# Kernel tuning notes

Hardware: AMD Instinct MI355X
Metric: run time of the kernel (lower is better)

Reference implementation:

```python
import jax, jax.numpy as jnp
import numpy as np

B, S, H, DH = 2, 2048, 16, 64
D = H * DH


def setup_inputs() -> dict:
    key = jax.random.key(0)
    ks = jax.random.split(key, 10)
    std = 0.02
    return {
        "hidden_states": jax.random.normal(ks[0], (B, S, D), jnp.float32),
        "mask": jax.random.randint(ks[1], (B, S), 0, 2, jnp.int64 if jax.config.jax_enable_x64 else jnp.int32),
        "Wq": jax.random.normal(ks[2], (D, D), jnp.float32) * std,
        "bq": jnp.zeros((D,), jnp.float32),
        "Wk": jax.random.normal(ks[3], (D, D), jnp.float32) * std,
        "bk": jnp.zeros((D,), jnp.float32),
        "Wv": jax.random.normal(ks[4], (D, D), jnp.float32) * std,
        "bv": jnp.zeros((D,), jnp.float32),
        "Wo": jax.random.normal(ks[5], (D, D), jnp.float32) * std,
        "bo": jnp.zeros((D,), jnp.float32),
    }


def _split_heads(x):
    # (B, S, H*DH) -> (B, H, S, DH)
    b, s, _ = x.shape
    return x.reshape(b, s, H, DH).transpose(0, 2, 1, 3)


def reference(hidden_states, mask, Wq, bq, Wk, bk, Wv, bv, Wo, bo):
    # Linear projections (torch nn.Linear: x @ W.T + b)
    q = _split_heads(hidden_states @ Wq.T + bq)
    k = _split_heads(hidden_states @ Wk.T + bk)
    v = _split_heads(hidden_states @ Wv.T + bv)

    scale = 1.0 / np.sqrt(DH).astype(np.float32)
    scores = jnp.einsum("bhqd,bhkd->bhqk", q, k) * scale  # (B,H,S,S)
    # mask out padded key positions (mask==0 -> -inf), broadcast over heads/queries
    scores = jnp.where(mask[:, None, None, :] == 0, -jnp.inf, scores)
    weights = jax.nn.softmax(scores, axis=-1)

    attended = jnp.einsum("bhqk,bhkd->bhqd", weights, v)  # (B,H,S,DH)
    merged = attended.transpose(0, 2, 1, 3).reshape(hidden_states.shape)  # (B,S,D)
    return merged @ Wo.T + bo
```

## Files before the change

### kernel.cpp

```cpp
#include <hip/hip_runtime.h>
#include <hip/hip_bf16.h>

typedef __bf16 bf16;
typedef __bf16 bf16x4 __attribute__((ext_vector_type(4)));
typedef __bf16 bf16x8 __attribute__((ext_vector_type(8)));
typedef float f32x4 __attribute__((ext_vector_type(4)));

#define B_ 2
#define S_ 2048
#define H_ 16
#define DH_ 64
#define D_ 1024
#define NT_ 4096

#define WAIT_VMCNT0() asm volatile("s_waitcnt vmcnt(0)" ::: "memory")
#define WAIT_LGKM0()  asm volatile("s_waitcnt lgkmcnt(0)" ::: "memory")

__device__ __forceinline__ void gld_lds16(const bf16* g, bf16* l) {
    __builtin_amdgcn_global_load_lds(
        (__attribute__((address_space(1))) void*)g,
        (__attribute__((address_space(3))) void*)l, 16, 0, 0);
}

__global__ __launch_bounds__(256) void cvt_kernel(
    const float* __restrict__ hs,
    const float* __restrict__ Wq, const float* __restrict__ Wk,
    const float* __restrict__ Wv, const float* __restrict__ Wo,
    bf16* __restrict__ hsb, bf16* __restrict__ wqkv, bf16* __restrict__ wob)
{
    int i = (blockIdx.x * 256 + threadIdx.x) * 4;
    const float* src;
    bf16* dst;
    if (i < 4194304) {
        src = hs + i; dst = hsb + i;
    } else if (i < 7340032) {
        int off = i - 4194304;
        int which = off >> 20;
        int within = off & 1048575;
        src = (which == 0 ? Wq : which == 1 ? Wk : Wv) + within;
        dst = wqkv + off;
    } else {
        int off = i - 7340032;
        src = Wo + off; dst = wob + off;
    }
    float4 v = *(const float4*)src;
    bf16x4 o = { (bf16)v.x, (bf16)v.y, (bf16)v.z, (bf16)v.w };
    *(bf16x4*)dst = o;
}

__global__ __launch_bounds__(256, 2) void gemm_bt(
    const bf16* __restrict__ A, const bf16* __restrict__ Bm,
    int mode,
    const float* __restrict__ b0, const float* __restrict__ b1,
    const float* __restrict__ b2,
    bf16* __restrict__ Qo, bf16* __restrict__ Ko, bf16* __restrict__ Vt,
    float* __restrict__ Co)
{
    const int K = 1024;
    __shared__ __attribute__((aligned(16))) bf16 sA[128 * 32];
    __shared__ __attribute__((aligned(16))) bf16 sB[128 * 32];

    int tid = threadIdx.x;
    int wave = tid >> 6, lane = tid & 63;
    int quad = lane >> 4, l16 = lane & 15;
    int m0 = blockIdx.x * 128;
    int n0 = blockIdx.y * 128;
    int wm = (wave & 1) * 64, wn = (wave >> 1) * 64;
    int fs = (l16 >> 1) & 3;

    f32x4 acc[4][4];
#pragma unroll
    for (int i = 0; i < 4; i++)
#pragma unroll
        for (int j = 0; j < 4; j++) acc[i][j] = (f32x4){0.f, 0.f, 0.f, 0.f};

    for (int k0 = 0; k0 < K; k0 += 32) {
#pragma unroll
        for (int i = 0; i < 2; i++) {
            int chunk = tid + i * 256;
            int row = chunk >> 2;
            int kc = ((chunk & 3) ^ ((row >> 1) & 3)) * 8;
            gld_lds16(A + (size_t)(m0 + row) * K + k0 + kc, &sA[chunk * 8]);
            gld_lds16(Bm + (size_t)(n0 + row) * K + k0 + kc, &sB[chunk * 8]);
        }
        WAIT_VMCNT0();
        __syncthreads();

        bf16x8 af[4], bfr[4];
#pragma unroll
        for (int i = 0; i < 4; i++)
            af[i] = *(const bf16x8*)&sA[(wm + i * 16 + l16) * 32 + (quad ^ fs) * 8];
#pragma unroll
        for (int j = 0; j < 4; j++)
            bfr[j] = *(const bf16x8*)&sB[(wn + j * 16 + l16) * 32 + (quad ^ fs) * 8];
#pragma unroll
        for (int i = 0; i < 4; i++)
#pragma unroll
            for (int j = 0; j < 4; j++)
                acc[i][j] = __builtin_amdgcn_mfma_f32_16x16x32_bf16(
                    af[i], bfr[j], acc[i][j], 0, 0, 0);
        WAIT_LGKM0();
        __syncthreads();
    }

    if (mode == 0) {
        const float QSCALE = 0.125f * 1.44269504088896340736f;
#pragma unroll
        for (int j = 0; j < 4; j++) {
            int n = n0 + wn + j * 16 + l16;
            int region = n >> 10;
            int nn = n & 1023;
            int h = nn >> 6, d = nn & 63;
            float bias = (region == 0 ? b0 : region == 1 ? b1 : b2)[nn];
#pragma unroll
            for (int i = 0; i < 4; i++)
#pragma unroll
                for (int r = 0; r < 4; r++) {
                    int m = m0 + wm + i * 16 + quad * 4 + r;
                    int b = m >> 11, s = m & 2047;
                    int bh = b * H_ + h;
                    float v = acc[i][j][r] + bias;
                    if (region == 0)
                        Qo[((size_t)bh * S_ + s) * DH_ + d] = (bf16)(v * QSCALE);
                    else if (region == 1)
                        Ko[((size_t)bh * S_ + s) * DH_ + d] = (bf16)v;
                    else
                        Vt[((size_t)bh * DH_ + d) * S_ + s] = (bf16)v;
                }
        }
    } else {
#pragma unroll
        for (int j = 0; j < 4; j++) {
            int n = n0 + wn + j * 16 + l16;
            float bias = b0[n];
#pragma unroll
            for (int i = 0; i < 4; i++)
#pragma unroll
                for (int r = 0; r < 4; r++) {
                    int m = m0 + wm + i * 16 + quad * 4 + r;
                    Co[(size_t)m * D_ + n] = acc[i][j][r] + bias;
                }
        }
    }
}

__global__ __launch_bounds__(256, 2) void attn_kernel(
    const bf16* __restrict__ Q, const bf16* __restrict__ Kg,
    const bf16* __restrict__ Vt, const int* __restrict__ mask,
    bf16* __restrict__ Og)
{
    __shared__ __attribute__((aligned(16))) bf16 sK[64 * 64];
    __shared__ __attribute__((aligned(16))) bf16 sV[64 * 64];
    __shared__ __attribute__((aligned(16))) bf16 sP[4][16 * 64];
    __shared__ float sMadd[64];

    int tid = threadIdx.x;
    int wave = tid >> 6, lane = tid & 63;
    int quad = lane >> 4, l16 = lane & 15;
    int bh = blockIdx.y;
    int b = bh >> 4;
    int q0 = blockIdx.x * 64;
    int f8 = l16 & 7;

    const bf16* Qb = Q + (size_t)bh * S_ * DH_;
    const bf16* Kb = Kg + (size_t)bh * S_ * DH_;
    const bf16* Vb = Vt + (size_t)bh * DH_ * S_;

    int qrow = q0 + wave * 16 + l16;
    bf16x8 aq0 = *(const bf16x8*)&Qb[(size_t)qrow * DH_ + quad * 8];
    bf16x8 aq1 = *(const bf16x8*)&Qb[(size_t)qrow * DH_ + 32 + quad * 8];

    f32x4 o[4];
#pragma unroll
    for (int i = 0; i < 4; i++) o[i] = (f32x4){0.f, 0.f, 0.f, 0.f};
    float psum[4] = {0.f, 0.f, 0.f, 0.f};

    for (int kt = 0; kt < S_; kt += 64) {
#pragma unroll
        for (int i = 0; i < 2; i++) {
            int chunk = tid + i * 256;
            int row = chunk >> 3;
            int cc = ((chunk & 7) ^ (row & 7)) * 8;
            gld_lds16(&Kb[(size_t)(kt + row) * DH_ + cc], &sK[chunk * 8]);
            gld_lds16(&Vb[(size_t)row * S_ + kt + cc], &sV[chunk * 8]);
        }
        if (tid < 64) sMadd[tid] = mask[b * S_ + kt + tid] ? 0.f : -1e30f;
        WAIT_VMCNT0();
        __syncthreads();

#pragma unroll
        for (int nt = 0; nt < 4; nt++) {
            bf16x8 bk0 = *(const bf16x8*)&sK[(nt * 16 + l16) * 64 + (quad ^ f8) * 8];
            bf16x8 bk1 = *(const bf16x8*)&sK[(nt * 16 + l16) * 64 + ((quad + 4) ^ f8) * 8];
            f32x4 c = (f32x4){0.f, 0.f, 0.f, 0.f};
            c = __builtin_amdgcn_mfma_f32_16x16x32_bf16(aq0, bk0, c, 0, 0, 0);
            c = __builtin_amdgcn_mfma_f32_16x16x32_bf16(aq1, bk1, c, 0, 0, 0);
            float ma = sMadd[nt * 16 + l16];
#pragma unroll
            for (int r = 0; r < 4; r++) {
                float p = exp2f(c[r] + ma);
                psum[r] += p;
                int row = quad * 4 + r;
                int g = (nt * 2 + (l16 >> 3)) ^ (row & 7);
                sP[wave][row * 64 + g * 8 + (l16 & 7)] = (bf16)p;
            }
        }

        WAIT_LGKM0();
        bf16x8 ap0 = *(const bf16x8*)&sP[wave][l16 * 64 + (quad ^ f8) * 8];
        bf16x8 ap1 = *(const bf16x8*)&sP[wave][l16 * 64 + ((quad + 4) ^ f8) * 8];
#pragma unroll
        for (int dt = 0; dt < 4; dt++) {
            bf16x8 bv0 = *(const bf16x8*)&sV[(dt * 16 + l16) * 64 + (quad ^ f8) * 8];
            bf16x8 bv1 = *(const bf16x8*)&sV[(dt * 16 + l16) * 64 + ((quad + 4) ^ f8) * 8];
            o[dt] = __builtin_amdgcn_mfma_f32_16x16x32_bf16(ap0, bv0, o[dt], 0, 0, 0);
            o[dt] = __builtin_amdgcn_mfma_f32_16x16x32_bf16(ap1, bv1, o[dt], 0, 0, 0);
        }
        WAIT_LGKM0();
        __syncthreads();
    }

    int h = bh & 15;
#pragma unroll
    for (int r = 0; r < 4; r++) {
        float v = psum[r];
        v += __shfl_xor(v, 1);
        v += __shfl_xor(v, 2);
        v += __shfl_xor(v, 4);
        v += __shfl_xor(v, 8);
        float rcp = 1.f / v;
        int s = q0 + wave * 16 + quad * 4 + r;
#pragma unroll
        for (int dt = 0; dt < 4; dt++) {
            int d = dt * 16 + l16;
            Og[((size_t)(b * S_ + s)) * D_ + h * 64 + d] = (bf16)(o[dt][r] * rcp);
        }
    }
}

extern "C" void kernel_launch(void* const* d_in, const int* in_sizes, int n_in,
                              void* d_out, int out_size, void* d_ws, size_t ws_size,
                              hipStream_t stream) {
    const float* hs = (const float*)d_in[0];
    const int* mask = (const int*)d_in[1];
    const float* Wq = (const float*)d_in[2];
    const float* bq = (const float*)d_in[3];
    const float* Wk = (const float*)d_in[4];
    const float* bk = (const float*)d_in[5];
    const float* Wv = (const float*)d_in[6];
    const float* bv = (const float*)d_in[7];
    const float* Wo = (const float*)d_in[8];
    const float* bo = (const float*)d_in[9];
    float* out = (float*)d_out;

    char* ws = (char*)d_ws;
    bf16* hsb  = (bf16*)(ws);
    bf16* wqkv = (bf16*)(ws + ((size_t)8 << 20));
    bf16* wob  = (bf16*)(ws + ((size_t)14 << 20));
    bf16* Qw   = (bf16*)(ws + ((size_t)16 << 20));
    bf16* Kw   = (bf16*)(ws + ((size_t)24 << 20));
    bf16* Vtw  = (bf16*)(ws + ((size_t)32 << 20));
    bf16* attn = (bf16*)(ws + ((size_t)40 << 20));

    cvt_kernel<<<8192, 256, 0, stream>>>(hs, Wq, Wk, Wv, Wo, hsb, wqkv, wob);
    gemm_bt<<<dim3(32, 24), 256, 0, stream>>>(hsb, wqkv, 0, bq, bk, bv,
                                              Qw, Kw, Vtw, nullptr);
    attn_kernel<<<dim3(32, 32), 256, 0, stream>>>(Qw, Kw, Vtw, mask, attn);
    gemm_bt<<<dim3(32, 8), 256, 0, stream>>>(attn, wob, 1, bo, nullptr, nullptr,
                                             nullptr, nullptr, nullptr, out);
}
```

Before: 225.0 us.

## Preload mask into LDS, raise attention occupancy, use fast exp2 and bf16 rounding

The attention kernel now loads the whole per-batch additive mask into shared memory once, instead of reloading 64 entries every key tile, and raises the launch-bounds occupancy hint from 2 to 4 blocks. It also uses the raw hardware exp2 intrinsic, replaces bf16 casts with a manual round-to-nearest-even bit trick, and drops redundant lgkmcnt waits before barriers. The larger shared array and the tighter register budget at higher occupancy risk register spills, and the fast exp2 drops denormal handling.

```diff
diff --git a/kernel.cpp b/kernel.cpp
--- a/kernel.cpp
+++ b/kernel.cpp
@@ -20,6 +20,12 @@
     __builtin_amdgcn_global_load_lds(
         (__attribute__((address_space(1))) void*)g,
         (__attribute__((address_space(3))) void*)l, 16, 0, 0);
+}
+
+__device__ __forceinline__ bf16 f2bf(float x) {
+    union { float f; unsigned u; } v; v.f = x;
+    unsigned short h = (unsigned short)((v.u + 0x7FFF + ((v.u >> 16) & 1)) >> 16);
+    return __builtin_bit_cast(bf16, h);
 }
 
 __global__ __launch_bounds__(256) void cvt_kernel(
@@ -99,7 +105,6 @@
             for (int j = 0; j < 4; j++)
                 acc[i][j] = __builtin_amdgcn_mfma_f32_16x16x32_bf16(
                     af[i], bfr[j], acc[i][j], 0, 0, 0);
-        WAIT_LGKM0();
         __syncthreads();
     }
 
@@ -121,11 +126,11 @@
                     int bh = b * H_ + h;
                     float v = acc[i][j][r] + bias;
                     if (region == 0)
-                        Qo[((size_t)bh * S_ + s) * DH_ + d] = (bf16)(v * QSCALE);
+                        Qo[((size_t)bh * S_ + s) * DH_ + d] = f2bf(v * QSCALE);
                     else if (region == 1)
-                        Ko[((size_t)bh * S_ + s) * DH_ + d] = (bf16)v;
+                        Ko[((size_t)bh * S_ + s) * DH_ + d] = f2bf(v);
                     else
-                        Vt[((size_t)bh * DH_ + d) * S_ + s] = (bf16)v;
+                        Vt[((size_t)bh * DH_ + d) * S_ + s] = f2bf(v);
                 }
         }
     } else {
@@ -144,7 +149,7 @@
     }
 }
 
-__global__ __launch_bounds__(256, 2) void attn_kernel(
+__global__ __launch_bounds__(256, 4) void attn_kernel(
     const bf16* __restrict__ Q, const bf16* __restrict__ Kg,
     const bf16* __restrict__ Vt, const int* __restrict__ mask,
     bf16* __restrict__ Og)
@@ -152,7 +157,7 @@
     __shared__ __attribute__((aligned(16))) bf16 sK[64 * 64];
     __shared__ __attribute__((aligned(16))) bf16 sV[64 * 64];
     __shared__ __attribute__((aligned(16))) bf16 sP[4][16 * 64];
-    __shared__ float sMadd[64];
+    __shared__ float sMaddAll[S_];
 
     int tid = threadIdx.x;
     int wave = tid >> 6, lane = tid & 63;
@@ -166,6 +171,12 @@
     const bf16* Kb = Kg + (size_t)bh * S_ * DH_;
     const bf16* Vb = Vt + (size_t)bh * DH_ * S_;
 
+#pragma unroll
+    for (int i = 0; i < S_ / 256; i++) {
+        int idx = tid + i * 256;
+        sMaddAll[idx] = mask[b * S_ + idx] ? 0.f : -1e30f;
+    }
+
     int qrow = q0 + wave * 16 + l16;
     bf16x8 aq0 = *(const bf16x8*)&Qb[(size_t)qrow * DH_ + quad * 8];
     bf16x8 aq1 = *(const bf16x8*)&Qb[(size_t)qrow * DH_ + 32 + quad * 8];
@@ -174,6 +185,8 @@
 #pragma unroll
     for (int i = 0; i < 4; i++) o[i] = (f32x4){0.f, 0.f, 0.f, 0.f};
     float psum[4] = {0.f, 0.f, 0.f, 0.f};
+
+    __syncthreads();
 
     for (int kt = 0; kt < S_; kt += 64) {
 #pragma unroll
@@ -184,7 +197,6 @@
             gld_lds16(&Kb[(size_t)(kt + row) * DH_ + cc], &sK[chunk * 8]);
             gld_lds16(&Vb[(size_t)row * S_ + kt + cc], &sV[chunk * 8]);
         }
-        if (tid < 64) sMadd[tid] = mask[b * S_ + kt + tid] ? 0.f : -1e30f;
         WAIT_VMCNT0();
         __syncthreads();
 
@@ -195,14 +207,14 @@
             f32x4 c = (f32x4){0.f, 0.f, 0.f, 0.f};
             c = __builtin_amdgcn_mfma_f32_16x16x32_bf16(aq0, bk0, c, 0, 0, 0);
             c = __builtin_amdgcn_mfma_f32_16x16x32_bf16(aq1, bk1, c, 0, 0, 0);
-            float ma = sMadd[nt * 16 + l16];
+            float ma = sMaddAll[kt + nt * 16 + l16];
 #pragma unroll
             for (int r = 0; r < 4; r++) {
-                float p = exp2f(c[r] + ma);
+                float p = __builtin_amdgcn_exp2f(c[r] + ma);
                 psum[r] += p;
                 int row = quad * 4 + r;
                 int g = (nt * 2 + (l16 >> 3)) ^ (row & 7);
-                sP[wave][row * 64 + g * 8 + (l16 & 7)] = (bf16)p;
+                sP[wave][row * 64 + g * 8 + (l16 & 7)] = f2bf(p);
             }
         }
 
@@ -216,7 +228,6 @@
             o[dt] = __builtin_amdgcn_mfma_f32_16x16x32_bf16(ap0, bv0, o[dt], 0, 0, 0);
             o[dt] = __builtin_amdgcn_mfma_f32_16x16x32_bf16(ap1, bv1, o[dt], 0, 0, 0);
         }
-        WAIT_LGKM0();
         __syncthreads();
     }
 
@@ -233,7 +244,7 @@
 #pragma unroll
         for (int dt = 0; dt < 4; dt++) {
             int d = dt * 16 + l16;
-            Og[((size_t)(b * S_ + s)) * D_ + h * 64 + d] = (bf16)(o[dt][r] * rcp);
+            Og[((size_t)(b * S_ + s)) * D_ + h * 64 + d] = f2bf(o[dt][r] * rcp);
         }
     }
 }
```

Measured after the change: 213.8 us. 5.0% less time.
